# Performance work log

Hardware: AMD Instinct MI355X
Metric: run time of the kernel (lower is better)

## Reference

```python
import jax, jax.numpy as jnp
import numpy as np

B, IN, H = 8192, 1024, 1024


def setup_inputs() -> dict:
    key = jax.random.key(0)
    ks = jax.random.split(key, 6)
    s = 1.0 / np.sqrt(H)
    return {
        "incoming": jax.random.normal(ks[0], (B, IN), dtype=jnp.float32),
        "state": jax.random.normal(ks[1], (2, B, H), dtype=jnp.float32),
        "Wx": jax.random.normal(ks[2], (4 * H, IN), dtype=jnp.float32) * s,
        "bx": jax.random.normal(ks[3], (4 * H,), dtype=jnp.float32) * s,
        "Wh": jax.random.normal(ks[4], (4 * H, H), dtype=jnp.float32) * s,
        "bh": jax.random.normal(ks[5], (4 * H,), dtype=jnp.float32) * s,
    }


def reference(incoming, state, Wx, bx, Wh, bh):
    # Fused form of 8 Linear layers: gates stacked in (i, f, g, o) order.
    h_prev, c_prev = state[0], state[1]
    gates = (jnp.einsum('bi,gi->bg', incoming, Wx) + bx
             + jnp.einsum('bh,gh->bg', h_prev, Wh) + bh)  # [B, 4H]
    i_g, f_g, g_g, o_g = jnp.split(gates, 4, axis=-1)
    i = jax.nn.sigmoid(i_g)
    f = jax.nn.sigmoid(f_g)
    g = jnp.tanh(g_g)
    o = jax.nn.sigmoid(o_g)
    new_c = f * c_prev + i * g
    new_h = o * jnp.tanh(new_c)
    # output == new_h; return stacked (new_h, new_c) as [2, B, H]
    return jnp.stack([new_h, new_c])
```

## Files before the change

### kernel.cpp

```cpp
#include <hip/hip_runtime.h>
#include <hip/hip_bf16.h>


#define B_DIM 8192
#define H_DIM 1024
#define BH (8192 * 1024)
#define K2 2048

typedef __attribute__((ext_vector_type(4))) float f32x4;
typedef __attribute__((ext_vector_type(8))) __bf16 bf16x8;
typedef __attribute__((ext_vector_type(8))) unsigned short ushort8;

static __device__ __forceinline__ unsigned short f2bf(float f) {
    return __builtin_bit_cast(unsigned short, (__bf16)f);
}
static __device__ __forceinline__ float sigf(float x) {
    return 1.0f / (1.0f + __expf(-x));
}
static __device__ __forceinline__ float tanhft(float x) {
    float e = __expf(2.0f * x);
    return (e - 1.0f) / (e + 1.0f);
}
static __device__ __forceinline__ void gload16(const void* g, void* l) {
    __builtin_amdgcn_global_load_lds(
        (const __attribute__((address_space(1))) unsigned int*)g,
        (__attribute__((address_space(3))) unsigned int*)l, 16, 0, 0);
}
static __device__ __forceinline__ ushort8 cvt8(const float* src) {
    const float4 u = ((const float4*)src)[0];
    const float4 v = ((const float4*)src)[1];
    ushort8 o;
    o[0] = f2bf(u.x); o[1] = f2bf(u.y); o[2] = f2bf(u.z); o[3] = f2bf(u.w);
    o[4] = f2bf(v.x); o[5] = f2bf(v.y); o[6] = f2bf(v.z); o[7] = f2bf(v.w);
    return o;
}

__global__ __launch_bounds__(256) void conv_kernel(
    const float* __restrict__ x, const float* __restrict__ h,
    const float* __restrict__ Wx, const float* __restrict__ Wh,
    unsigned short* __restrict__ A, unsigned short* __restrict__ W)
{
    const int bidx = blockIdx.x;
    if (bidx < 8192) {
        const int id = bidx * 256 + threadIdx.x;
        const int base = id * 8;
        const int b = base >> 11;
        const int k = base & 2047;
        const float* src = (k < 1024) ? (x + (size_t)b * 1024 + k)
                                      : (h + (size_t)b * 1024 + (k - 1024));
        *(ushort8*)(A + base) = cvt8(src);
    } else {
        const int id = (bidx - 8192) * 256 + threadIdx.x;
        const int base = id * 8;
        const int n = base >> 11;
        const int k = base & 2047;
        const int jb = n >> 8, wn = (n >> 6) & 3, g = (n >> 4) & 3, jj = n & 15;
        const int srow = (g << 10) + (jb << 6) + (wn << 4) + jj;
        const float* src = (k < 1024) ? (Wx + (size_t)srow * 1024 + k)
                                      : (Wh + (size_t)srow * 1024 + (k - 1024));
        *(ushort8*)(W + base) = cvt8(src);
    }
}

__global__ __launch_bounds__(512, 2) void lstm_gemm8(
    const unsigned short* __restrict__ Abf, const unsigned short* __restrict__ Wbf,
    const float* __restrict__ bx, const float* __restrict__ bh,
    const float* __restrict__ cprev, float* __restrict__ out)
{
    extern __shared__ unsigned short lds[];

    const int tid = threadIdx.x;
    const int lane = tid & 63;
    const int wv = tid >> 6;
    const int wm = wv >> 2;
    const int wn = wv & 3;
    const int q = lane >> 4, c = lane & 15;

    const int bid = blockIdx.x;
    const int wg = (bid & 7) * 64 + (bid >> 3);
    const int bb = wg >> 4;
    const int jb = wg & 15;
    const int b0 = bb * 256;

    const unsigned short* Ab = Abf + (size_t)b0 * K2;
    const unsigned short* Wb = Wbf + (size_t)(jb * 256) * K2;

    const int srow = tid >> 2;
    const int sk8g = (tid & 3) ^ ((tid >> 3) & 3);
    const size_t ss0 = (size_t)srow * K2 + (size_t)sk8g * 8;
    const unsigned sdst = (unsigned)(tid & 448) * 8;

    const int cq = ((q ^ ((c >> 1) & 3)) << 3);
    const unsigned aoff = (unsigned)(wm * 128 + c) * 32 + cq;
    const unsigned boff = 16384u + (unsigned)(wn * 64 + c) * 32 + cq;

    f32x4 acc[8][4];
#pragma unroll
    for (int m = 0; m < 8; ++m)
#pragma unroll
        for (int g = 0; g < 4; ++g) acc[m][g] = f32x4{0.f, 0.f, 0.f, 0.f};

    bf16x8 av[4], bv[4];

#define STAGE(TP, T, ISB, KS) do {                                             \
    const unsigned short* _s = (ISB) ? Wb : Ab;                                \
    const size_t _o = ss0 + (size_t)((T) & 31) * 64 + (KS) * 32;               \
    const unsigned _d = ((TP) << 15) | ((ISB) << 14) | ((KS) << 13);           \
    gload16(_s + _o, &lds[_d + sdst]);                                         \
    gload16(_s + (size_t)128 * K2 + _o, &lds[_d + 4096u + sdst]);              \
} while (0)

#define LOADA(BUF, KS, MH) do {                                                \
    const unsigned short* _p = lds + (BUF) * 32768 + (KS) * 8192 + aoff + (MH) * 2048; \
    av[0] = *(const bf16x8*)(_p);                                              \
    av[1] = *(const bf16x8*)(_p + 512);                                        \
    av[2] = *(const bf16x8*)(_p + 1024);                                       \
    av[3] = *(const bf16x8*)(_p + 1536);                                       \
} while (0)

#define LOADB(BUF, KS) do {                                                    \
    const unsigned short* _p = lds + (BUF) * 32768 + (KS) * 8192 + boff;       \
    bv[0] = *(const bf16x8*)(_p);                                              \
    bv[1] = *(const bf16x8*)(_p + 512);                                        \
    bv[2] = *(const bf16x8*)(_p + 1024);                                       \
    bv[3] = *(const bf16x8*)(_p + 1536);                                       \
} while (0)

#define MFMA16(MH) do {                                                        \
    __builtin_amdgcn_s_setprio(1);                                             \
    _Pragma("unroll")                                                          \
    for (int _i = 0; _i < 4; ++_i)                                             \
        _Pragma("unroll")                                                      \
        for (int _g = 0; _g < 4; ++_g)                                         \
            acc[(MH) * 4 + _i][_g] = __builtin_amdgcn_mfma_f32_16x16x32_bf16(  \
                av[_i], bv[_g], acc[(MH) * 4 + _i][_g], 0, 0, 0);              \
    __builtin_amdgcn_s_setprio(0);                                             \
} while (0)

#define BAR_SOFT() __builtin_amdgcn_s_barrier()
#define BAR_FENCE() asm volatile("s_barrier" ::: "memory")
#define WAIT_LGKM() asm volatile("s_waitcnt lgkmcnt(0)" ::: "memory")
#define WAIT_VM4() asm volatile("s_waitcnt vmcnt(4)" ::: "memory")

#define PH(BUF, KS, MH, RB, STP, ST, SB, SK) do {                              \
    LOADA(BUF, KS, MH);                                                        \
    if (RB) LOADB(BUF, KS);                                                    \
    STAGE(STP, ST, SB, SK);                                                    \
    BAR_SOFT();                                                                \
    WAIT_LGKM();                                                               \
    MFMA16(MH);                                                                \
    BAR_FENCE();                                                               \
} while (0)

#define PHV(BUF, KS, MH, STP, ST, SB, SK) do {                                 \
    LOADA(BUF, KS, MH);                                                        \
    STAGE(STP, ST, SB, SK);                                                    \
    BAR_SOFT();                                                                \
    WAIT_LGKM();                                                               \
    MFMA16(MH);                                                                \
    WAIT_VM4();                                                                \
    BAR_FENCE();                                                               \
} while (0)

    STAGE(0, 0, 0, 0); STAGE(0, 0, 1, 0); STAGE(0, 0, 0, 1); STAGE(0, 0, 1, 1);
    STAGE(1, 1, 0, 0); STAGE(1, 1, 1, 0);
    WAIT_VM4();
    BAR_FENCE();

    for (int u = 0; u < 32; u += 2) {
        PH (0, 0, 0, 1, 1, u + 1, 0, 1);
        PH (0, 0, 1, 0, 1, u + 1, 1, 1);
        PH (0, 1, 0, 1, 0, u + 2, 0, 0);
        PHV(0, 1, 1,    0, u + 2, 1, 0);
        PH (1, 0, 0, 1, 0, u + 2, 0, 1);
        PH (1, 0, 1, 0, 0, u + 2, 1, 1);
        PH (1, 1, 0, 1, 1, u + 3, 0, 0);
        PHV(1, 1, 1,    1, u + 3, 1, 0);
    }

#undef PH
#undef PHV
#undef STAGE
#undef LOADA
#undef LOADB
#undef MFMA16

    const int j = jb * 64 + wn * 16 + c;
    const float bI = bx[j] + bh[j];
    const float bF = bx[1024 + j] + bh[1024 + j];
    const float bG = bx[2048 + j] + bh[2048 + j];
    const float bO = bx[3072 + j] + bh[3072 + j];
#pragma unroll
    for (int mt = 0; mt < 8; ++mt) {
#pragma unroll
        for (int rr = 0; rr < 4; ++rr) {
            const int row = b0 + wm * 128 + mt * 16 + q * 4 + rr;
            const size_t off = (size_t)row * 1024 + j;
            const float iv = sigf(acc[mt][0][rr] + bI);
            const float fv = sigf(acc[mt][1][rr] + bF);
            const float gv = tanhft(acc[mt][2][rr] + bG);
            const float ov = sigf(acc[mt][3][rr] + bO);
            const float cp = cprev[off];
            const float nc = fv * cp + iv * gv;
            out[off] = ov * tanhft(nc);
            out[BH + off] = nc;
        }
    }
}

__global__ __launch_bounds__(256) void lstm_fallback(
    const float* __restrict__ incoming, const float* __restrict__ state,
    const float* __restrict__ Wx, const float* __restrict__ bx,
    const float* __restrict__ Wh, const float* __restrict__ bh,
    float* __restrict__ out)
{
    __shared__ unsigned short lA[128 * 64];
    __shared__ unsigned short lW[128 * 64];
    const int t = threadIdx.x;
    const int lane = t & 63;
    const int wv = t >> 6;
    const int q = lane >> 4;
    const int c = lane & 15;
    const int j0 = blockIdx.x * 32;
    const int b0 = blockIdx.y * 128;
    const float* hprev = state;
    const float* cprev = state + (size_t)BH;

    f32x4 acc[2][8];
#pragma unroll
    for (int mt = 0; mt < 2; ++mt)
#pragma unroll
        for (int nt = 0; nt < 8; ++nt)
            acc[mt][nt] = f32x4{0.f, 0.f, 0.f, 0.f};

    const int sr = t >> 3;
    const int sk8 = t & 7;

    for (int it = 0; it < 32; ++it) {
        const bool first = (it < 16);
        const float* As = first ? incoming : hprev;
        const float* Ws = first ? Wx : Wh;
        const int kk = first ? it * 64 : it * 64 - 1024;
#pragma unroll
        for (int i = 0; i < 4; ++i) {
            const int r = i * 32 + sr;
            *(ushort8*)&lA[r * 64 + ((sk8 ^ (r & 7)) * 8)] =
                cvt8(As + (size_t)(b0 + r) * 1024 + kk + sk8 * 8);
        }
#pragma unroll
        for (int i = 0; i < 4; ++i) {
            const int n = i * 32 + sr;
            const int grow = ((n >> 5) << 10) + j0 + (n & 31);
            *(ushort8*)&lW[n * 64 + ((sk8 ^ (n & 7)) * 8)] =
                cvt8(Ws + (size_t)grow * 1024 + kk + sk8 * 8);
        }
        __syncthreads();
#pragma unroll
        for (int ks = 0; ks < 2; ++ks) {
            const int k8a = ks * 4 + q;
            bf16x8 av[2], bv[8];
#pragma unroll
            for (int mt = 0; mt < 2; ++mt) {
                const int r = wv * 32 + mt * 16 + c;
                av[mt] = *(const bf16x8*)&lA[r * 64 + ((k8a ^ (r & 7)) * 8)];
            }
#pragma unroll
            for (int nt = 0; nt < 8; ++nt) {
                const int n = nt * 16 + c;
                bv[nt] = *(const bf16x8*)&lW[n * 64 + ((k8a ^ (n & 7)) * 8)];
            }
#pragma unroll
            for (int mt = 0; mt < 2; ++mt)
#pragma unroll
                for (int nt = 0; nt < 8; ++nt)
                    acc[mt][nt] = __builtin_amdgcn_mfma_f32_16x16x32_bf16(
                        av[mt], bv[nt], acc[mt][nt], 0, 0, 0);
        }
        __syncthreads();
    }

    const int b0r = b0 + wv * 32;
#pragma unroll
    for (int jt = 0; jt < 2; ++jt) {
        const int j = j0 + jt * 16 + c;
        const float bI = bx[j] + bh[j];
        const float bF = bx[1024 + j] + bh[1024 + j];
        const float bG = bx[2048 + j] + bh[2048 + j];
        const float bO = bx[3072 + j] + bh[3072 + j];
#pragma unroll
        for (int mt = 0; mt < 2; ++mt) {
#pragma unroll
            for (int rr = 0; rr < 4; ++rr) {
                const int row = b0r + mt * 16 + q * 4 + rr;
                const size_t off = (size_t)row * 1024 + j;
                const float iv = sigf(acc[mt][0 + jt][rr] + bI);
                const float fv = sigf(acc[mt][2 + jt][rr] + bF);
                const float gv = tanhft(acc[mt][4 + jt][rr] + bG);
                const float ov = sigf(acc[mt][6 + jt][rr] + bO);
                const float cp = cprev[off];
                const float nc = fv * cp + iv * gv;
                out[off] = ov * tanhft(nc);
                out[BH + off] = nc;
            }
        }
    }
}

extern "C" void kernel_launch(void* const* d_in, const int* in_sizes, int n_in,
                              void* d_out, int out_size, void* d_ws, size_t ws_size,
                              hipStream_t stream) {
    const float* incoming = (const float*)d_in[0];
    const float* state    = (const float*)d_in[1];
    const float* Wx       = (const float*)d_in[2];
    const float* bx       = (const float*)d_in[3];
    const float* Wh       = (const float*)d_in[4];
    const float* bh       = (const float*)d_in[5];
    float* out = (float*)d_out;

    const float* hprev = state;
    const float* cprev = state + (size_t)BH;

    const size_t A_bytes = (size_t)B_DIM * K2 * 2;
    const size_t W_bytes = (size_t)4 * H_DIM * K2 * 2;

    if (ws_size >= A_bytes + W_bytes) {
        unsigned short* Abf = (unsigned short*)d_ws;
        unsigned short* Wbf = (unsigned short*)((char*)d_ws + A_bytes);
        conv_kernel<<<dim3(12288), dim3(256), 0, stream>>>(
            incoming, hprev, Wx, Wh, Abf, Wbf);
        (void)hipFuncSetAttribute((const void*)lstm_gemm8,
                                  hipFuncAttributeMaxDynamicSharedMemorySize, 131072);
        lstm_gemm8<<<dim3(512), dim3(512), 131072, stream>>>(
            Abf, Wbf, bx, bh, cprev, out);
    } else {
        dim3 grid(H_DIM / 32, B_DIM / 128);
        lstm_fallback<<<grid, dim3(256), 0, stream>>>(
            incoming, state, Wx, bx, Wh, bh, out);
    }
}
```

Measured before the change: 165.4 us.

## Remap workgroups to XCDs by weight column and relax barrier memory clobbers

Changes the block-to-tile mapping so that each XCD handles two fixed weight column blocks and iterates over batch blocks, instead of the previous interleaved mapping. The aim is better L2 reuse of the weight tiles within each XCD. It also removes the memory clobbers from the barrier and lgkmcnt wait asm so the compiler has more scheduling freedom. Dropping those clobbers risks the compiler reordering LDS accesses across the barriers.

Result: no change. 166.8 us (+0.8%).

```diff
diff --git a/kernel.cpp b/kernel.cpp
--- a/kernel.cpp
+++ b/kernel.cpp
@@ -77,9 +77,10 @@
     const int q = lane >> 4, c = lane & 15;
 
     const int bid = blockIdx.x;
-    const int wg = (bid & 7) * 64 + (bid >> 3);
-    const int bb = wg >> 4;
-    const int jb = wg & 15;
+    const int xcd = bid & 7;
+    const int idx = bid >> 3;
+    const int jb  = xcd * 2 + (idx & 1);
+    const int bb  = idx >> 1;
     const int b0 = bb * 256;
 
     const unsigned short* Ab = Abf + (size_t)b0 * K2;
@@ -137,35 +138,34 @@
     __builtin_amdgcn_s_setprio(0);                                             \
 } while (0)
 
-#define BAR_SOFT() __builtin_amdgcn_s_barrier()
-#define BAR_FENCE() asm volatile("s_barrier" ::: "memory")
-#define WAIT_LGKM() asm volatile("s_waitcnt lgkmcnt(0)" ::: "memory")
-#define WAIT_VM4() asm volatile("s_waitcnt vmcnt(4)" ::: "memory")
+#define BAR()    __builtin_amdgcn_s_barrier()
+#define WLGKM0() asm volatile("s_waitcnt lgkmcnt(0)")
+#define WVM4()   asm volatile("s_waitcnt vmcnt(4)" ::: "memory")
 
 #define PH(BUF, KS, MH, RB, STP, ST, SB, SK) do {                              \
     LOADA(BUF, KS, MH);                                                        \
     if (RB) LOADB(BUF, KS);                                                    \
     STAGE(STP, ST, SB, SK);                                                    \
-    BAR_SOFT();                                                                \
-    WAIT_LGKM();                                                               \
+    BAR();                                                                     \
+    WLGKM0();                                                                  \
     MFMA16(MH);                                                                \
-    BAR_FENCE();                                                               \
+    BAR();                                                                     \
 } while (0)
 
 #define PHV(BUF, KS, MH, STP, ST, SB, SK) do {                                 \
     LOADA(BUF, KS, MH);                                                        \
     STAGE(STP, ST, SB, SK);                                                    \
-    BAR_SOFT();                                                                \
-    WAIT_LGKM();                                                               \
+    BAR();                                                                     \
+    WLGKM0();                                                                  \
     MFMA16(MH);                                                                \
-    WAIT_VM4();                                                                \
-    BAR_FENCE();                                                               \
+    WVM4();                                                                    \
+    BAR();                                                                     \
 } while (0)
 
     STAGE(0, 0, 0, 0); STAGE(0, 0, 1, 0); STAGE(0, 0, 0, 1); STAGE(0, 0, 1, 1);
     STAGE(1, 1, 0, 0); STAGE(1, 1, 1, 0);
-    WAIT_VM4();
-    BAR_FENCE();
+    WVM4();
+    BAR();
 
     for (int u = 0; u < 32; u += 2) {
         PH (0, 0, 0, 1, 1, u + 1, 0, 1);
```
